# Kernel optimization log

Measured on AMD Instinct MI355X. Metric: run time of the kernel, lower is better.

## Reference

```python
import jax, jax.numpy as jnp
import numpy as np

IN1, IN2, OUT = 256, 64, 64

def setup_inputs() -> dict:
    key = jax.random.key(0)
    k1, k2, k3, k4 = jax.random.split(key, 4)
    x1 = jax.random.normal(k1, (4, 4096, IN1), dtype=jnp.float32)
    x2 = jax.random.normal(k2, (4, 4096, IN2), dtype=jnp.float32)
    # nn.Linear(in_1, in_2*out): weight (in_2*out, in_1), bias (in_2*out,)
    W = jax.random.normal(k3, (IN2 * OUT, IN1), dtype=jnp.float32) / np.sqrt(IN1)
    bvec = jax.random.normal(k4, (IN2 * OUT,), dtype=jnp.float32) * 0.01
    return {"x1": x1, "x2": x2, "W": W, "bvec": bvec}

def reference(x1, x2, W, bvec):
    b, n, _ = x1.shape
    # per-token generated weight: (b, n, in_2, out)
    w = (jnp.einsum('bni,oi->bno', x1, W) + bvec).reshape(b, n, IN2, OUT)
    # batched vector-matrix product per token
    y = jnp.einsum('bnj,bnjo->bno', x2, w)
    return y
```

## Files before the change

kernel.cpp:

```cpp
#include <hip/hip_runtime.h>


#define FRAG_SHORTS 512
#define JSTEP (2 * 16 * FRAG_SHORTS)
#define BIAS_OFF ((size_t)(64 * 2 * 16) * FRAG_SHORTS)

typedef __bf16 bf16x8 __attribute__((ext_vector_type(8)));
typedef float  f32x16 __attribute__((ext_vector_type(16)));

static __device__ __forceinline__ unsigned short f2bf(float f) {
  union { float f; unsigned u; } v; v.f = f;
  unsigned r = v.u + 0x7FFFu + ((v.u >> 16) & 1u);
  return (unsigned short)(r >> 16);
}

static __device__ __forceinline__ bf16x8 pack8(float4 a, float4 b) {
  union { bf16x8 v; unsigned short u[8]; } r;
  r.u[0] = f2bf(a.x); r.u[1] = f2bf(a.y); r.u[2] = f2bf(a.z); r.u[3] = f2bf(a.w);
  r.u[4] = f2bf(b.x); r.u[5] = f2bf(b.y); r.u[6] = f2bf(b.z); r.u[7] = f2bf(b.w);
  return r.v;
}

static __device__ __forceinline__ void gload_lds16(const unsigned short* g,
                                                   unsigned short* l) {
  __builtin_amdgcn_global_load_lds(
      (const __attribute__((address_space(1))) void*)g,
      (__attribute__((address_space(3))) void*)l, 16, 0, 0);
}

__global__ void prep_w(const float* __restrict__ W, const float* __restrict__ bv,
                       unsigned short* __restrict__ Wf) {
  int idx = blockIdx.x * 256 + threadIdx.x;
  int r  = idx >> 4;
  int ks = idx & 15;
  int j   = r >> 6;
  int o   = r & 63;
  int oh  = o >> 5;
  int l31 = o & 31;
  size_t fb = ((size_t)(j * 2 + oh) * 16 + ks) * FRAG_SHORTS;

  const float4* row = (const float4*)(W + (size_t)r * 256 + ks * 16);
  float4 v0 = row[0], v1 = row[1], v2 = row[2], v3 = row[3];
  ushort4 lo0, lo1, hi0, hi1;
  lo0.x = f2bf(v0.x); lo0.y = f2bf(v0.y); lo0.z = f2bf(v0.z); lo0.w = f2bf(v0.w);
  lo1.x = f2bf(v1.x); lo1.y = f2bf(v1.y); lo1.z = f2bf(v1.z); lo1.w = f2bf(v1.w);
  hi0.x = f2bf(v2.x); hi0.y = f2bf(v2.y); hi0.z = f2bf(v2.z); hi0.w = f2bf(v2.w);
  hi1.x = f2bf(v3.x); hi1.y = f2bf(v3.y); hi1.z = f2bf(v3.z); hi1.w = f2bf(v3.w);
  *(ushort4*)&Wf[fb + l31 * 8 + 0] = lo0;
  *(ushort4*)&Wf[fb + l31 * 8 + 4] = lo1;
  *(ushort4*)&Wf[fb + 256 + l31 * 8 + 0] = hi0;
  *(ushort4*)&Wf[fb + 256 + l31 * 8 + 4] = hi1;

  if (idx < 512) {
    int f   = idx >> 6;
    int ln  = idx & 63;
    int ohb = f >> 2, jq = f & 3;
    int lb  = ln & 31, lgb = ln >> 5;
    #pragma unroll
    for (int e = 0; e < 8; ++e)
      Wf[BIAS_OFF + (size_t)f * FRAG_SHORTS + ln * 8 + e] =
          f2bf(bv[(jq * 16 + 8 * lgb + e) * 64 + 32 * ohb + lb]);
  }
}

__global__
__attribute__((amdgpu_flat_work_group_size(512, 512), amdgpu_waves_per_eu(2, 2)))
void meta_main(const float* __restrict__ x1, const float* __restrict__ x2,
               const unsigned short* __restrict__ Wf, float* __restrict__ out) {
  __shared__ __align__(16) unsigned char smem[163840];
  float* sX2 = (float*)smem;
  unsigned short* ringS = (unsigned short*)(smem + 32768);
  float* red = (float*)(smem + 32768);

  const int tid  = threadIdx.x;
  const int lane = tid & 63;
  const int wv   = tid >> 6;
  const int kh   = wv & 3;
  const int jh   = wv >> 2;
  const int l31  = lane & 31;
  const int lg   = lane >> 5;

  const int bid  = blockIdx.x;
  const int oh   = bid & 1;
  const long tile0 = (long)(bid >> 1) * 128;

  {
    const float4* s2 = (const float4*)(x2 + tile0 * 64);
    #pragma unroll
    for (int it = 0; it < 4; ++it) {
      int fi4 = it * 512 + tid;
      float4 v = s2[fi4];
      int token = fi4 >> 4;
      int j0    = (fi4 & 15) * 4;
      sX2[(j0 + 0) * 128 + token] = v.x;
      sX2[(j0 + 1) * 128 + token] = v.y;
      sX2[(j0 + 2) * 128 + token] = v.z;
      sX2[(j0 + 3) * 128 + token] = v.w;
    }
  }

  bf16x8 bf[4][4];
  #pragma unroll
  for (int m = 0; m < 4; ++m) {
    #pragma unroll
    for (int q = 0; q < 4; ++q) {
      const float* p = x1 + (size_t)(tile0 + m * 32 + l31) * 256 +
                       (kh * 4 + q) * 16 + lg * 8;
      bf[m][q] = pack8(*(const float4*)p, *(const float4*)(p + 4));
    }
  }
  __syncthreads();

  f32x16 z;
  #pragma unroll
  for (int r = 0; r < 16; ++r) z[r] = 0.0f;

  f32x16 y[4];
  #pragma unroll
  for (int m = 0; m < 4; ++m) y[m] = z;
  if (kh == 0) {
    #pragma unroll
    for (int qq = 0; qq < 2; ++qq) {
      int jq = jh * 2 + qq;
      bf16x8 bias = *(const bf16x8*)(Wf + BIAS_OFF +
                                     (size_t)(oh * 4 + jq) * FRAG_SHORTS + lane * 8);
      #pragma unroll
      for (int m = 0; m < 4; ++m) {
        union { bf16x8 v; unsigned short u[8]; } xf;
        #pragma unroll
        for (int e = 0; e < 8; ++e)
          xf.u[e] = f2bf(sX2[(jq * 16 + 8 * lg + e) * 128 + m * 32 + l31]);
        y[m] = __builtin_amdgcn_mfma_f32_32x32x16_bf16(bias, xf.v, y[m], 0, 0, 0);
      }
    }
  }
  __syncthreads();

  const int fragsel = jh * 8192 + (kh * 4) * 512;
  unsigned short* lds_w = ringS + fragsel;
  const unsigned short* rd_w = ringS + fragsel + lane * 8;
  const unsigned short* gsrc0 =
      Wf + (size_t)jh * 32 * JSTEP + (size_t)(oh * 16 + kh * 4) * FRAG_SHORTS + lane * 8;

#define STAGE(T, SLOT)                                                          \
  {                                                                             \
    const unsigned short* gs = gsrc0 + (size_t)(T) * JSTEP;                     \
    unsigned short* ls = lds_w + (SLOT) * 16384;                                \
    gload_lds16(gs + 0 * 512, ls + 0 * 512);                                    \
    gload_lds16(gs + 1 * 512, ls + 1 * 512);                                    \
    gload_lds16(gs + 2 * 512, ls + 2 * 512);                                    \
    gload_lds16(gs + 3 * 512, ls + 3 * 512);                                    \
  }

  STAGE(0, 0);
  STAGE(1, 1);

  #pragma unroll 4
  for (int p = 0; p < 32; ++p) {
    STAGE((p + 2) & 31, (p + 2) & 3);
    asm volatile("s_waitcnt vmcnt(8)" ::: "memory");
    __builtin_amdgcn_s_barrier();

    const unsigned short* rb = rd_w + (p & 3) * 16384;
    bf16x8 w0 = *(const bf16x8*)(rb + 0 * 512);
    bf16x8 w1 = *(const bf16x8*)(rb + 1 * 512);
    bf16x8 w2 = *(const bf16x8*)(rb + 2 * 512);
    bf16x8 w3 = *(const bf16x8*)(rb + 3 * 512);
    const int jg = jh * 32 + p;

    f32x16 aA, aB;
    __builtin_amdgcn_s_setprio(1);
    aA = __builtin_amdgcn_mfma_f32_32x32x16_bf16(w0, bf[0][0], z, 0, 0, 0);
    aB = __builtin_amdgcn_mfma_f32_32x32x16_bf16(w0, bf[1][0], z, 0, 0, 0);
    aA = __builtin_amdgcn_mfma_f32_32x32x16_bf16(w1, bf[0][1], aA, 0, 0, 0);
    aB = __builtin_amdgcn_mfma_f32_32x32x16_bf16(w1, bf[1][1], aB, 0, 0, 0);
    aA = __builtin_amdgcn_mfma_f32_32x32x16_bf16(w2, bf[0][2], aA, 0, 0, 0);
    aB = __builtin_amdgcn_mfma_f32_32x32x16_bf16(w2, bf[1][2], aB, 0, 0, 0);
    aA = __builtin_amdgcn_mfma_f32_32x32x16_bf16(w3, bf[0][3], aA, 0, 0, 0);
    aB = __builtin_amdgcn_mfma_f32_32x32x16_bf16(w3, bf[1][3], aB, 0, 0, 0);
    __builtin_amdgcn_s_setprio(0);
    {
      float xs0 = sX2[jg * 128 + l31];
      float xs1 = sX2[jg * 128 + 32 + l31];
      #pragma unroll
      for (int r = 0; r < 16; ++r) {
        y[0][r] += xs0 * aA[r];
        y[1][r] += xs1 * aB[r];
      }
    }
    __builtin_amdgcn_s_setprio(1);
    aA = __builtin_amdgcn_mfma_f32_32x32x16_bf16(w0, bf[2][0], z, 0, 0, 0);
    aB = __builtin_amdgcn_mfma_f32_32x32x16_bf16(w0, bf[3][0], z, 0, 0, 0);
    aA = __builtin_amdgcn_mfma_f32_32x32x16_bf16(w1, bf[2][1], aA, 0, 0, 0);
    aB = __builtin_amdgcn_mfma_f32_32x32x16_bf16(w1, bf[3][1], aB, 0, 0, 0);
    aA = __builtin_amdgcn_mfma_f32_32x32x16_bf16(w2, bf[2][2], aA, 0, 0, 0);
    aB = __builtin_amdgcn_mfma_f32_32x32x16_bf16(w2, bf[3][2], aB, 0, 0, 0);
    aA = __builtin_amdgcn_mfma_f32_32x32x16_bf16(w3, bf[2][3], aA, 0, 0, 0);
    aB = __builtin_amdgcn_mfma_f32_32x32x16_bf16(w3, bf[3][3], aB, 0, 0, 0);
    __builtin_amdgcn_s_setprio(0);
    {
      float xs2 = sX2[jg * 128 + 64 + l31];
      float xs3 = sX2[jg * 128 + 96 + l31];
      #pragma unroll
      for (int r = 0; r < 16; ++r) {
        y[2][r] += xs2 * aA[r];
        y[3][r] += xs3 * aB[r];
      }
    }
  }
#undef STAGE

  __syncthreads();

#define RED_W(S)                                                   \
  { float* b = red + (S) * 4352;                                   \
    _Pragma("unroll") for (int m = 0; m < 4; ++m)                  \
      _Pragma("unroll") for (int r = 0; r < 16; ++r)               \
        b[(m * 64 + lane) * 17 + r] = y[m][r]; }
#define RED_A(S)                                                   \
  { const float* b = red + (S) * 4352;                             \
    _Pragma("unroll") for (int m = 0; m < 4; ++m)                  \
      _Pragma("unroll") for (int r = 0; r < 16; ++r)               \
        y[m][r] += b[(m * 64 + lane) * 17 + r]; }

  if (kh >= 2) RED_W((kh - 2) * 2 + jh);
  __syncthreads();
  if (kh < 2)  RED_A(kh * 2 + jh);
  __syncthreads();
  if (kh == 1) RED_W(jh);
  __syncthreads();
  if (kh == 0) RED_A(jh);
  __syncthreads();
  if (kh == 0 && jh == 1) RED_W(0);
  __syncthreads();
  if (wv == 0) {
    RED_A(0);
    #pragma unroll
    for (int m = 0; m < 4; ++m) {
      float* yo = out + (tile0 + m * 32 + l31) * 64 + oh * 32;
      #pragma unroll
      for (int rq = 0; rq < 4; ++rq) {
        float4 v = make_float4(y[m][4 * rq + 0], y[m][4 * rq + 1],
                               y[m][4 * rq + 2], y[m][4 * rq + 3]);
        *(float4*)(yo + 8 * rq + 4 * lg) = v;
      }
    }
  }
#undef RED_W
#undef RED_A
}

extern "C" void kernel_launch(void* const* d_in, const int* in_sizes, int n_in,
                              void* d_out, int out_size, void* d_ws, size_t ws_size,
                              hipStream_t stream) {
  const float* x1 = (const float*)d_in[0];
  const float* x2 = (const float*)d_in[1];
  const float* W  = (const float*)d_in[2];
  const float* bv = (const float*)d_in[3];
  float* y = (float*)d_out;
  unsigned short* Wf = (unsigned short*)d_ws;

  prep_w<<<256, 256, 0, stream>>>(W, bv, Wf);
  meta_main<<<256, 512, 0, stream>>>(x1, x2, Wf, y);
}
```

Before: 113.9 us.

## Software-pipeline LDS weight reads into registers and drop per-step barrier

Restructures the main loop to process two j-steps per iteration and to issue the LDS reads of the next weight fragments before the current step's MFMA block, using ping-pong register sets. The global-to-LDS prefetch distance grows from two stages to three, the per-iteration workgroup barrier is removed, and the s_setprio hints are dropped. The goal is to hide LDS read latency behind MFMAs and to cut synchronisation stalls. In exchange it uses more VGPRs and relies on each wave reading only the LDS slots it loaded itself. There is also a possible hazard when a ring slot is overwritten shortly after it was read.

```diff
diff --git a/kernel.cpp b/kernel.cpp
--- a/kernel.cpp
+++ b/kernel.cpp
@@ -152,63 +152,71 @@
     gload_lds16(gs + 3 * 512, ls + 3 * 512);                                    \
   }
 
+#define DSREAD(D0, D1, D2, D3, SLOT)                                            \
+  {                                                                             \
+    const unsigned short* rb = rd_w + (SLOT) * 16384;                           \
+    D0 = *(const bf16x8*)(rb + 0 * 512);                                        \
+    D1 = *(const bf16x8*)(rb + 1 * 512);                                        \
+    D2 = *(const bf16x8*)(rb + 2 * 512);                                        \
+    D3 = *(const bf16x8*)(rb + 3 * 512);                                        \
+  }
+
+#define MFMABLK(W0, W1, W2, W3, P)                                              \
+  {                                                                             \
+    const int jg = jh * 32 + (P);                                               \
+    float xs0 = sX2[jg * 128 + l31];                                            \
+    float xs1 = sX2[jg * 128 + 32 + l31];                                       \
+    float xs2 = sX2[jg * 128 + 64 + l31];                                       \
+    float xs3 = sX2[jg * 128 + 96 + l31];                                       \
+    f32x16 aA, aB;                                                              \
+    aA = __builtin_amdgcn_mfma_f32_32x32x16_bf16(W0, bf[0][0], z, 0, 0, 0);     \
+    aB = __builtin_amdgcn_mfma_f32_32x32x16_bf16(W0, bf[1][0], z, 0, 0, 0);     \
+    aA = __builtin_amdgcn_mfma_f32_32x32x16_bf16(W1, bf[0][1], aA, 0, 0, 0);    \
+    aB = __builtin_amdgcn_mfma_f32_32x32x16_bf16(W1, bf[1][1], aB, 0, 0, 0);    \
+    aA = __builtin_amdgcn_mfma_f32_32x32x16_bf16(W2, bf[0][2], aA, 0, 0, 0);    \
+    aB = __builtin_amdgcn_mfma_f32_32x32x16_bf16(W2, bf[1][2], aB, 0, 0, 0);    \
+    aA = __builtin_amdgcn_mfma_f32_32x32x16_bf16(W3, bf[0][3], aA, 0, 0, 0);    \
+    aB = __builtin_amdgcn_mfma_f32_32x32x16_bf16(W3, bf[1][3], aB, 0, 0, 0);    \
+    _Pragma("unroll")                                                           \
+    for (int r = 0; r < 16; ++r) {                                              \
+      y[0][r] += xs0 * aA[r];                                                   \
+      y[1][r] += xs1 * aB[r];                                                   \
+    }                                                                           \
+    aA = __builtin_amdgcn_mfma_f32_32x32x16_bf16(W0, bf[2][0], z, 0, 0, 0);     \
+    aB = __builtin_amdgcn_mfma_f32_32x32x16_bf16(W0, bf[3][0], z, 0, 0, 0);     \
+    aA = __builtin_amdgcn_mfma_f32_32x32x16_bf16(W1, bf[2][1], aA, 0, 0, 0);    \
+    aB = __builtin_amdgcn_mfma_f32_32x32x16_bf16(W1, bf[3][1], aB, 0, 0, 0);    \
+    aA = __builtin_amdgcn_mfma_f32_32x32x16_bf16(W2, bf[2][2], aA, 0, 0, 0);    \
+    aB = __builtin_amdgcn_mfma_f32_32x32x16_bf16(W2, bf[3][2], aB, 0, 0, 0);    \
+    aA = __builtin_amdgcn_mfma_f32_32x32x16_bf16(W3, bf[2][3], aA, 0, 0, 0);    \
+    aB = __builtin_amdgcn_mfma_f32_32x32x16_bf16(W3, bf[3][3], aB, 0, 0, 0);    \
+    _Pragma("unroll")                                                           \
+    for (int r = 0; r < 16; ++r) {                                              \
+      y[2][r] += xs2 * aA[r];                                                   \
+      y[3][r] += xs3 * aB[r];                                                   \
+    }                                                                           \
+  }
+
+  bf16x8 c0, c1, c2, c3, r0, r1, r2, r3;
   STAGE(0, 0);
   STAGE(1, 1);
-
-  #pragma unroll 4
-  for (int p = 0; p < 32; ++p) {
-    STAGE((p + 2) & 31, (p + 2) & 3);
+  STAGE(2, 2);
+  asm volatile("s_waitcnt vmcnt(8)" ::: "memory");
+  DSREAD(c0, c1, c2, c3, 0);
+
+  for (int p = 0; p < 32; p += 2) {
+    STAGE((p + 3) & 31, (p + 3) & 3);
     asm volatile("s_waitcnt vmcnt(8)" ::: "memory");
-    __builtin_amdgcn_s_barrier();
-
-    const unsigned short* rb = rd_w + (p & 3) * 16384;
-    bf16x8 w0 = *(const bf16x8*)(rb + 0 * 512);
-    bf16x8 w1 = *(const bf16x8*)(rb + 1 * 512);
-    bf16x8 w2 = *(const bf16x8*)(rb + 2 * 512);
-    bf16x8 w3 = *(const bf16x8*)(rb + 3 * 512);
-    const int jg = jh * 32 + p;
-
-    f32x16 aA, aB;
-    __builtin_amdgcn_s_setprio(1);
-    aA = __builtin_amdgcn_mfma_f32_32x32x16_bf16(w0, bf[0][0], z, 0, 0, 0);
-    aB = __builtin_amdgcn_mfma_f32_32x32x16_bf16(w0, bf[1][0], z, 0, 0, 0);
-    aA = __builtin_amdgcn_mfma_f32_32x32x16_bf16(w1, bf[0][1], aA, 0, 0, 0);
-    aB = __builtin_amdgcn_mfma_f32_32x32x16_bf16(w1, bf[1][1], aB, 0, 0, 0);
-    aA = __builtin_amdgcn_mfma_f32_32x32x16_bf16(w2, bf[0][2], aA, 0, 0, 0);
-    aB = __builtin_amdgcn_mfma_f32_32x32x16_bf16(w2, bf[1][2], aB, 0, 0, 0);
-    aA = __builtin_amdgcn_mfma_f32_32x32x16_bf16(w3, bf[0][3], aA, 0, 0, 0);
-    aB = __builtin_amdgcn_mfma_f32_32x32x16_bf16(w3, bf[1][3], aB, 0, 0, 0);
-    __builtin_amdgcn_s_setprio(0);
-    {
-      float xs0 = sX2[jg * 128 + l31];
-      float xs1 = sX2[jg * 128 + 32 + l31];
-      #pragma unroll
-      for (int r = 0; r < 16; ++r) {
-        y[0][r] += xs0 * aA[r];
-        y[1][r] += xs1 * aB[r];
-      }
-    }
-    __builtin_amdgcn_s_setprio(1);
-    aA = __builtin_amdgcn_mfma_f32_32x32x16_bf16(w0, bf[2][0], z, 0, 0, 0);
-    aB = __builtin_amdgcn_mfma_f32_32x32x16_bf16(w0, bf[3][0], z, 0, 0, 0);
-    aA = __builtin_amdgcn_mfma_f32_32x32x16_bf16(w1, bf[2][1], aA, 0, 0, 0);
-    aB = __builtin_amdgcn_mfma_f32_32x32x16_bf16(w1, bf[3][1], aB, 0, 0, 0);
-    aA = __builtin_amdgcn_mfma_f32_32x32x16_bf16(w2, bf[2][2], aA, 0, 0, 0);
-    aB = __builtin_amdgcn_mfma_f32_32x32x16_bf16(w2, bf[3][2], aB, 0, 0, 0);
-    aA = __builtin_amdgcn_mfma_f32_32x32x16_bf16(w3, bf[2][3], aA, 0, 0, 0);
-    aB = __builtin_amdgcn_mfma_f32_32x32x16_bf16(w3, bf[3][3], aB, 0, 0, 0);
-    __builtin_amdgcn_s_setprio(0);
-    {
-      float xs2 = sX2[jg * 128 + 64 + l31];
-      float xs3 = sX2[jg * 128 + 96 + l31];
-      #pragma unroll
-      for (int r = 0; r < 16; ++r) {
-        y[2][r] += xs2 * aA[r];
-        y[3][r] += xs3 * aB[r];
-      }
-    }
+    DSREAD(r0, r1, r2, r3, (p + 1) & 3);
+    MFMABLK(c0, c1, c2, c3, p);
+    STAGE((p + 4) & 31, (p + 4) & 3);
+    asm volatile("s_waitcnt vmcnt(8)" ::: "memory");
+    DSREAD(c0, c1, c2, c3, (p + 2) & 3);
+    MFMABLK(r0, r1, r2, r3, p + 1);
   }
 #undef STAGE
+#undef DSREAD
+#undef MFMABLK
 
   __syncthreads();
 
```

Result: no change. 115.5 us (+1.4%).
